# Kernel tuning notes

Measured on AMD Instinct MI355X. Metric: run time of the kernel, lower is better.

## Reference

```python
import jax, jax.numpy as jnp
import numpy as np

N = 200000
HID = 256
HEADS = 8
HD = HID // HEADS
C = 1000  # num clusters


def setup_inputs() -> dict:
    key = jax.random.key(0)
    ks = jax.random.split(key, 8)
    s = 1.0 / np.sqrt(HID)
    return {
        "x": jax.random.normal(ks[0], (N, HID), dtype=jnp.float32),
        "cluster_assignments": jax.random.randint(ks[1], (N,), 0, C),
        "batch": jnp.zeros((N,), dtype=jnp.int64),
        "Wk": jax.random.uniform(ks[2], (HID, HID), minval=-s, maxval=s),
        "bk": jnp.zeros((HID,), dtype=jnp.float32),
        "Wv": jax.random.uniform(ks[3], (HID, HID), minval=-s, maxval=s),
        "bv": jnp.zeros((HID,), dtype=jnp.float32),
        "Wo": jax.random.uniform(ks[4], (HID, HID), minval=-s, maxval=s),
        "bo": jnp.zeros((HID,), dtype=jnp.float32),
        "pool_query": jax.random.normal(ks[5], (1, HEADS, HD), dtype=jnp.float32),
    }


def reference(x, cluster_assignments, batch, Wk, bk, Wv, bv, Wo, bo, pool_query):
    seg = cluster_assignments
    scale = HD ** -0.5
    keys = (x @ Wk.T + bk).reshape(-1, HEADS, HD)     # [N, H, D]
    values = (x @ Wv.T + bv).reshape(-1, HEADS, HD)   # [N, H, D]
    # attention scores per node/head against shared pool query
    scores = jnp.einsum('nhd,hd->nh', keys, pool_query[0]) * scale  # [N, H]
    # segment-wise (per-cluster) softmax over nodes, per head
    m = jax.ops.segment_max(scores, seg, num_segments=C)            # [C, H]
    e = jnp.exp(scores - m[seg])                                    # [N, H]
    z = jax.ops.segment_sum(e, seg, num_segments=C)                 # [C, H]
    w = e / z[seg]                                                  # [N, H]
    attended = (w[..., None] * values).reshape(-1, HID)             # [N, HID]
    # scatter_mean over clusters
    ssum = jax.ops.segment_sum(attended, seg, num_segments=C)       # [C, HID]
    cnt = jax.ops.segment_sum(jnp.ones((attended.shape[0],), attended.dtype), seg, num_segments=C)
    pooled = ssum / jnp.clip(cnt, 1.0)[:, None]                     # [C, HID]
    out = pooled @ Wo.T + bo                                        # [C, HID]
    return out[seg]                                                 # [N, HID]
```

## Files before the change

### kernel.cpp

```cpp
#include <hip/hip_runtime.h>
#include <math.h>

#define HID 256
#define HEADS 8
#define HD 32
#define C_CLUST 1000
#define SCALEQ 0.17677669529663687f
#define CAP 512
#define NW 8

__global__ __launch_bounds__(256) void k_prep(const float* __restrict__ Wk,
                                              const float* __restrict__ bk,
                                              const float* __restrict__ pq,
                                              float* __restrict__ qk,
                                              float* __restrict__ cb,
                                              int* __restrict__ cur) {
  __shared__ float qv[HD];
  int h = blockIdx.x;
  int t = threadIdx.x;
  int g = h * 256 + t;
  for (int i = g; i < C_CLUST; i += 2048) cur[i] = 0;
  if (t < HD) qv[t] = pq[h * HD + t];
  __syncthreads();
  float a = 0.f;
#pragma unroll 8
  for (int d = 0; d < HD; ++d) a += Wk[(size_t)(h * HD + d) * HID + t] * qv[d];
  qk[h * HID + t] = a * SCALEQ;
  if (t == 0) {
    float s = 0.f;
    for (int d = 0; d < HD; ++d) s += bk[h * HD + d] * qv[d];
    cb[h] = s * SCALEQ;
  }
}

__global__ __launch_bounds__(256) void k_scores(const float* __restrict__ x,
                                                const int* __restrict__ seg,
                                                const float* __restrict__ qk,
                                                const float* __restrict__ cb,
                                                float* __restrict__ es,
                                                int* __restrict__ cur,
                                                int* __restrict__ list, int N) {
  int l = threadIdx.x & 63;
  int wid = (int)(((size_t)blockIdx.x * blockDim.x + threadIdx.x) >> 6);
  int nw = (int)(((size_t)gridDim.x * blockDim.x) >> 6);
  float4 q4[8];
#pragma unroll
  for (int h = 0; h < 8; ++h) q4[h] = *(const float4*)(qk + h * HID + 4 * l);
  float cbv = cb[l & 7];
#pragma unroll 2
  for (int n = wid; n < N; n += nw) {
    float4 xv = *(const float4*)(x + (size_t)n * HID + 4 * l);
    float r0 = xv.x * q4[0].x + xv.y * q4[0].y + xv.z * q4[0].z + xv.w * q4[0].w;
    float r1 = xv.x * q4[1].x + xv.y * q4[1].y + xv.z * q4[1].z + xv.w * q4[1].w;
    float r2 = xv.x * q4[2].x + xv.y * q4[2].y + xv.z * q4[2].z + xv.w * q4[2].w;
    float r3 = xv.x * q4[3].x + xv.y * q4[3].y + xv.z * q4[3].z + xv.w * q4[3].w;
    float r4 = xv.x * q4[4].x + xv.y * q4[4].y + xv.z * q4[4].z + xv.w * q4[4].w;
    float r5 = xv.x * q4[5].x + xv.y * q4[5].y + xv.z * q4[5].z + xv.w * q4[5].w;
    float r6 = xv.x * q4[6].x + xv.y * q4[6].y + xv.z * q4[6].z + xv.w * q4[6].w;
    float r7 = xv.x * q4[7].x + xv.y * q4[7].y + xv.z * q4[7].z + xv.w * q4[7].w;
    r0 += __shfl_xor(r0, 1); r0 += __shfl_xor(r0, 2); r0 += __shfl_xor(r0, 4);
    r1 += __shfl_xor(r1, 1); r1 += __shfl_xor(r1, 2); r1 += __shfl_xor(r1, 4);
    r2 += __shfl_xor(r2, 1); r2 += __shfl_xor(r2, 2); r2 += __shfl_xor(r2, 4);
    r3 += __shfl_xor(r3, 1); r3 += __shfl_xor(r3, 2); r3 += __shfl_xor(r3, 4);
    r4 += __shfl_xor(r4, 1); r4 += __shfl_xor(r4, 2); r4 += __shfl_xor(r4, 4);
    r5 += __shfl_xor(r5, 1); r5 += __shfl_xor(r5, 2); r5 += __shfl_xor(r5, 4);
    r6 += __shfl_xor(r6, 1); r6 += __shfl_xor(r6, 2); r6 += __shfl_xor(r6, 4);
    r7 += __shfl_xor(r7, 1); r7 += __shfl_xor(r7, 2); r7 += __shfl_xor(r7, 4);
    int p = l & 7;
    float v = (p < 4) ? ((p < 2) ? (p == 0 ? r0 : r1) : (p == 2 ? r2 : r3))
                      : ((p < 6) ? (p == 4 ? r4 : r5) : (p == 6 ? r6 : r7));
    v += __shfl_xor(v, 8); v += __shfl_xor(v, 16); v += __shfl_xor(v, 32);
    v += cbv;
    if (l < 8) es[(size_t)n * 8 + l] = __expf(v);
    if (l == 0) {
      int c = seg[n];
      int pos = atomicAdd(&cur[c], 1);
      if (pos < CAP) list[c * CAP + pos] = n;
    }
  }
}

__global__ __launch_bounds__(512) void k_pool(const float* __restrict__ x,
                                              const float* __restrict__ es,
                                              const int* __restrict__ cur,
                                              const int* __restrict__ list,
                                              const float* __restrict__ Wv,
                                              const float* __restrict__ bv,
                                              const float* __restrict__ Wo,
                                              const float* __restrict__ bo,
                                              float* __restrict__ outc) {
  __shared__ float4 buf4[512];
  __shared__ float s_lds[8 * HID];
  __shared__ float red[NW * 8];
  __shared__ float p_lds[HID];
  int c = blockIdx.x;
  int t = threadIdx.x;
  int cnt = cur[c];
  if (cnt == 0) return;
  int cntL = (cnt < CAP) ? cnt : CAP;
  int w = t >> 6, l = t & 63;
  const int* lp = list + c * CAP;

  float4 acc[8];
#pragma unroll
  for (int h = 0; h < 8; ++h) acc[h] = make_float4(0.f, 0.f, 0.f, 0.f);
  float zacc[8];
#pragma unroll
  for (int h = 0; h < 8; ++h) zacc[h] = 0.f;
  const float* xb = x + 4 * l;

#define ROW(NI)                                                                \
  { int nn = (NI);                                                             \
    float4 ea = *(const float4*)(es + (size_t)nn * 8);                         \
    float4 eb4 = *(const float4*)(es + (size_t)nn * 8 + 4);                    \
    float4 xv = *(const float4*)(xb + (size_t)nn * HID);                       \
    float eh[8] = {ea.x, ea.y, ea.z, ea.w, eb4.x, eb4.y, eb4.z, eb4.w};        \
    _Pragma("unroll")                                                          \
    for (int h = 0; h < 8; ++h) {                                              \
      acc[h].x += eh[h] * xv.x; acc[h].y += eh[h] * xv.y;                      \
      acc[h].z += eh[h] * xv.z; acc[h].w += eh[h] * xv.w;                      \
      zacc[h] += eh[h]; } }
  int i = w;
  for (; i + 3 * NW < cntL; i += 4 * NW) {
    int n0 = lp[i], n1 = lp[i + NW], n2 = lp[i + 2 * NW], n3 = lp[i + 3 * NW];
    ROW(n0) ROW(n1) ROW(n2) ROW(n3)
  }
  for (; i < cntL; i += NW) ROW(lp[i])
#undef ROW

#pragma unroll
  for (int h = 0; h < 8; ++h)
    if (l == h) red[w * 8 + h] = zacc[h];
  __syncthreads();
  float zinv[8];
#pragma unroll
  for (int h = 0; h < 8; ++h) {
    float z = 0.f;
#pragma unroll
    for (int w2 = 0; w2 < NW; ++w2) z += red[w2 * 8 + h];
    zinv[h] = (z > 0.f) ? 1.f / z : 0.f;
  }

#pragma unroll
  for (int h = 0; h < 8; ++h) {
    __syncthreads();
    buf4[t] = acc[h];
    __syncthreads();
    if (t < 64) {
      float4 s = buf4[t];
#pragma unroll
      for (int w2 = 1; w2 < NW; ++w2) {
        float4 b = buf4[w2 * 64 + t];
        s.x += b.x; s.y += b.y; s.z += b.z; s.w += b.w;
      }
      float sc = zinv[h];
      s.x *= sc; s.y *= sc; s.z *= sc; s.w *= sc;
      *(float4*)&s_lds[h * HID + 4 * t] = s;
    }
  }
  __syncthreads();

  int grp = t >> 2, q = t & 3;
  float rc = 1.f / (float)cnt;
#pragma unroll
  for (int r = 0; r < 2; ++r) {
    int o = grp + 128 * r;
    const float4* wr = (const float4*)(Wv + (size_t)o * HID);
    const float4* sr = (const float4*)(s_lds + (o >> 5) * HID);
    float a = 0.f;
#pragma unroll
    for (int k = 0; k < 16; ++k) {
      float4 w4 = wr[q + 4 * k];
      float4 s4 = sr[q + 4 * k];
      a += w4.x * s4.x + w4.y * s4.y + w4.z * s4.z + w4.w * s4.w;
    }
    a += __shfl_xor(a, 1);
    a += __shfl_xor(a, 2);
    if (q == 0) p_lds[o] = (a + bv[o]) * rc;
  }
  __syncthreads();
#pragma unroll
  for (int r = 0; r < 2; ++r) {
    int o = grp + 128 * r;
    const float4* wr = (const float4*)(Wo + (size_t)o * HID);
    const float4* pr = (const float4*)p_lds;
    float a = 0.f;
#pragma unroll
    for (int k = 0; k < 16; ++k) {
      float4 w4 = wr[q + 4 * k];
      float4 p4 = pr[q + 4 * k];
      a += w4.x * p4.x + w4.y * p4.y + w4.z * p4.z + w4.w * p4.w;
    }
    a += __shfl_xor(a, 1);
    a += __shfl_xor(a, 2);
    if (q == 0) outc[(size_t)c * HID + o] = a + bo[o];
  }
}

__global__ __launch_bounds__(256) void k_expand(const int* __restrict__ seg,
                                                const float* __restrict__ outc,
                                                float* __restrict__ out, int N) {
  size_t g = (size_t)blockIdx.x * blockDim.x + threadIdx.x;
  size_t total = (size_t)N * (HID / 4);
  size_t stride = (size_t)gridDim.x * blockDim.x;
  const float4* oc = (const float4*)outc;
  float4* o4 = (float4*)out;
  for (; g < total; g += stride) {
    int n = (int)(g >> 6);
    int q = (int)(g & 63);
    int c = seg[n];
    o4[g] = oc[(size_t)c * 64 + q];
  }
}

extern "C" void kernel_launch(void* const* d_in, const int* in_sizes, int n_in,
                              void* d_out, int out_size, void* d_ws, size_t ws_size,
                              hipStream_t stream) {
  const float* x = (const float*)d_in[0];
  const int* seg = (const int*)d_in[1];
  const float* Wk = (const float*)d_in[3];
  const float* bk = (const float*)d_in[4];
  const float* Wv = (const float*)d_in[5];
  const float* bv = (const float*)d_in[6];
  const float* Wo = (const float*)d_in[7];
  const float* bo = (const float*)d_in[8];
  const float* pq = (const float*)d_in[9];
  int N = in_sizes[0] / HID;

  char* ws = (char*)d_ws;
  size_t cur_off = 0;
  auto take = [&](size_t bytes) -> void* {
    void* p = ws + cur_off;
    cur_off += (bytes + 255) & ~(size_t)255;
    return p;
  };
  float* qk = (float*)take((size_t)HEADS * HID * 4);
  float* cb = (float*)take((size_t)HEADS * 4);
  int* cur = (int*)take((size_t)C_CLUST * 4);
  int* list = (int*)take((size_t)C_CLUST * CAP * 4);
  float* es = (float*)take((size_t)N * 8 * 4);
  float* outc = (float*)take((size_t)C_CLUST * HID * 4);

  k_prep<<<HEADS, 256, 0, stream>>>(Wk, bk, pq, qk, cb, cur);
  int sb = (N + 31) / 32;
  k_scores<<<sb, 256, 0, stream>>>(x, seg, qk, cb, es, cur, list, N);
  k_pool<<<C_CLUST, 512, 0, stream>>>(x, es, cur, list, Wv, bv, Wo, bo, outc);
  k_expand<<<2048, 256, 0, stream>>>(seg, outc, (float*)d_out, N);
}
```

Baseline: 185.8 us.

## Fuse cluster output expansion into pooling kernel with nontemporal stores

Removes the separate expand kernel. Each pooling block now writes its cluster's output row directly to every member node using the gathered node list and nontemporal stores. This saves a launch, the intermediate per-cluster buffer and the per-element segment lookups. It also deepens the accumulation unroll from 4 to 8 rows per wave. Output writes now depend on the list, so nodes beyond CAP in an overflowing cluster would not be written. Only 1000 blocks do the 205MB write, which may limit write parallelism.

```diff
diff --git a/kernel.cpp b/kernel.cpp
--- a/kernel.cpp
+++ b/kernel.cpp
@@ -8,6 +8,8 @@
 #define SCALEQ 0.17677669529663687f
 #define CAP 512
 #define NW 8
+
+typedef float fx4 __attribute__((ext_vector_type(4)));
 
 __global__ __launch_bounds__(256) void k_prep(const float* __restrict__ Wk,
                                               const float* __restrict__ bk,
@@ -88,11 +90,12 @@
                                               const float* __restrict__ bv,
                                               const float* __restrict__ Wo,
                                               const float* __restrict__ bo,
-                                              float* __restrict__ outc) {
+                                              float* __restrict__ out) {
   __shared__ float4 buf4[512];
   __shared__ float s_lds[8 * HID];
   __shared__ float red[NW * 8];
   __shared__ float p_lds[HID];
+  __shared__ float orow[HID];
   int c = blockIdx.x;
   int t = threadIdx.x;
   int cnt = cur[c];
@@ -121,9 +124,11 @@
       acc[h].z += eh[h] * xv.z; acc[h].w += eh[h] * xv.w;                      \
       zacc[h] += eh[h]; } }
   int i = w;
-  for (; i + 3 * NW < cntL; i += 4 * NW) {
-    int n0 = lp[i], n1 = lp[i + NW], n2 = lp[i + 2 * NW], n3 = lp[i + 3 * NW];
-    ROW(n0) ROW(n1) ROW(n2) ROW(n3)
+  for (; i + 7 * NW < cntL; i += 8 * NW) {
+    int n0 = lp[i],          n1 = lp[i + NW],     n2 = lp[i + 2 * NW],
+        n3 = lp[i + 3 * NW], n4 = lp[i + 4 * NW], n5 = lp[i + 5 * NW],
+        n6 = lp[i + 6 * NW], n7 = lp[i + 7 * NW];
+    ROW(n0) ROW(n1) ROW(n2) ROW(n3) ROW(n4) ROW(n5) ROW(n6) ROW(n7)
   }
   for (; i < cntL; i += NW) ROW(lp[i])
 #undef ROW
@@ -193,23 +198,14 @@
     }
     a += __shfl_xor(a, 1);
     a += __shfl_xor(a, 2);
-    if (q == 0) outc[(size_t)c * HID + o] = a + bo[o];
-  }
-}
-
-__global__ __launch_bounds__(256) void k_expand(const int* __restrict__ seg,
-                                                const float* __restrict__ outc,
-                                                float* __restrict__ out, int N) {
-  size_t g = (size_t)blockIdx.x * blockDim.x + threadIdx.x;
-  size_t total = (size_t)N * (HID / 4);
-  size_t stride = (size_t)gridDim.x * blockDim.x;
-  const float4* oc = (const float4*)outc;
-  float4* o4 = (float4*)out;
-  for (; g < total; g += stride) {
-    int n = (int)(g >> 6);
-    int q = (int)(g & 63);
-    int c = seg[n];
-    o4[g] = oc[(size_t)c * 64 + q];
+    if (q == 0) orow[o] = a + bo[o];
+  }
+  __syncthreads();
+
+  fx4 ov = *(const fx4*)&orow[4 * l];
+  for (int j = w; j < cntL; j += NW) {
+    int n = lp[j];
+    __builtin_nontemporal_store(ov, (fx4*)(out + (size_t)n * HID + 4 * l));
   }
 }
 
@@ -239,11 +235,10 @@
   int* cur = (int*)take((size_t)C_CLUST * 4);
   int* list = (int*)take((size_t)C_CLUST * CAP * 4);
   float* es = (float*)take((size_t)N * 8 * 4);
-  float* outc = (float*)take((size_t)C_CLUST * HID * 4);
 
   k_prep<<<HEADS, 256, 0, stream>>>(Wk, bk, pq, qk, cb, cur);
   int sb = (N + 31) / 32;
   k_scores<<<sb, 256, 0, stream>>>(x, seg, qk, cb, es, cur, list, N);
-  k_pool<<<C_CLUST, 512, 0, stream>>>(x, es, cur, list, Wv, bv, Wo, bo, outc);
-  k_expand<<<2048, 256, 0, stream>>>(seg, outc, (float*)d_out, N);
-}
+  k_pool<<<C_CLUST, 512, 0, stream>>>(x, es, cur, list, Wv, bv, Wo, bo,
+                                      (float*)d_out);
+}
```

New measurement: 204.2 us. 9.9% more time.
